# Kernel optimization log

Hardware: AMD Instinct MI355X
Metric: run time of the kernel (lower is better)

Reference implementation:

```python
import jax, jax.numpy as jnp
import numpy as np
from jax import lax

EPS = 1e-5
NUM_GROUPS = 32
OFFSET_SCALE = 1.0
K = 3            # deformable conv kernel size
KK = K * K
DWK = 7          # depthwise kernel size for offset predictor


def group_norm(x, gamma, beta, num_groups=NUM_GROUPS):
    B, C, H, W = x.shape
    xg = x.reshape(B, num_groups, C // num_groups, H, W)
    m = xg.mean(axis=(2, 3, 4), keepdims=True)
    v = xg.var(axis=(2, 3, 4), keepdims=True)
    xn = ((xg - m) * lax.rsqrt(v + EPS)).reshape(B, C, H, W)
    return xn * gamma[None, :, None, None] + beta[None, :, None, None]


def bilinear_gather(x, py, px):
    # x: [B,C,H,W]; py, px: [B,KK,H,W] absolute sample coords -> [B,C,KK,H,W]
    B, C, H, W = x.shape
    y0 = jnp.floor(py)
    x0 = jnp.floor(px)
    wy1 = py - y0
    wx1 = px - x0
    wy0 = 1.0 - wy1
    wx0 = 1.0 - wx1
    xf = x.reshape(B, C, H * W)

    def gather(yi, xi):
        valid = (yi >= 0) & (yi <= H - 1) & (xi >= 0) & (xi <= W - 1)
        yc = jnp.clip(yi, 0, H - 1).astype(jnp.int32)
        xc = jnp.clip(xi, 0, W - 1).astype(jnp.int32)
        idx = (yc * W + xc).reshape(B, -1)                      # [B, KK*H*W]
        g = jax.vmap(lambda a, i: a[:, i])(xf, idx)             # [B, C, KK*H*W]
        g = g.reshape(B, C, KK, H, W)
        return g * valid.astype(x.dtype)[:, None]

    out = (gather(y0, x0) * (wy0 * wx0)[:, None]
           + gather(y0, x0 + 1.0) * (wy0 * wx1)[:, None]
           + gather(y0 + 1.0, x0) * (wy1 * wx0)[:, None]
           + gather(y0 + 1.0, x0 + 1.0) * (wy1 * wx1)[:, None])
    return out


def deform_conv(x, dw, pw, pwb, w, b):
    # x: [B,C,H,W]; dw: [C,1,DWK,DWK] depthwise; pw: [2*KK,C,1,1]; w: [O,C,K,K]
    B, C, H, W = x.shape
    dn = ('NCHW', 'OIHW', 'NCHW')
    f = lax.conv_general_dilated(x, dw, (1, 1), 'SAME',
                                 feature_group_count=C, dimension_numbers=dn)
    off = lax.conv_general_dilated(f, pw, (1, 1), 'SAME', dimension_numbers=dn)
    off = (off + pwb[None, :, None, None]) * OFFSET_SCALE       # [B,2*KK,H,W]
    off = off.reshape(B, KK, 2, H, W)
    ks = jnp.arange(K, dtype=x.dtype) - (K - 1) / 2             # [-1,0,1]
    ky = jnp.repeat(ks, K)                                      # [KK]
    kx = jnp.tile(ks, K)
    yy, xx = jnp.meshgrid(jnp.arange(H, dtype=x.dtype),
                          jnp.arange(W, dtype=x.dtype), indexing='ij')
    py = yy[None, None] + ky[None, :, None, None] + off[:, :, 0]  # [B,KK,H,W]
    px = xx[None, None] + kx[None, :, None, None] + off[:, :, 1]
    sampled = bilinear_gather(x, py, px)                        # [B,C,KK,H,W]
    O = w.shape[0]
    out = jnp.einsum('bckhw,ock->bohw', sampled, w.reshape(O, C, KK))
    return out + b[None, :, None, None]


def setup_inputs() -> dict:
    key = jax.random.key(0)
    ks = jax.random.split(key, 10)
    B, C, H, W = 4, 256, 64, 64
    O = C
    x = jax.random.normal(ks[0], (B, C, H, W), dtype=jnp.float32)

    def conv_w(k, shape, fan_in):
        return jax.random.normal(k, shape, dtype=jnp.float32) / np.sqrt(fan_in)

    inp = {
        'x': x,
        'gn1_g': jnp.ones((C,), jnp.float32), 'gn1_b': jnp.zeros((C,), jnp.float32),
        'dw1': conv_w(ks[1], (C, 1, DWK, DWK), DWK * DWK),
        'pw1': jax.random.normal(ks[2], (2 * KK, C, 1, 1), jnp.float32) * 0.01,
        'pwb1': jnp.zeros((2 * KK,), jnp.float32),
        'w1': conv_w(ks[3], (O, C, K, K), C * KK),
        'b1': jnp.zeros((O,), jnp.float32),
        'gn2_g': jnp.ones((O,), jnp.float32), 'gn2_b': jnp.zeros((O,), jnp.float32),
        'dw2': conv_w(ks[4], (O, 1, DWK, DWK), DWK * DWK),
        'pw2': jax.random.normal(ks[5], (2 * KK, O, 1, 1), jnp.float32) * 0.01,
        'pwb2': jnp.zeros((2 * KK,), jnp.float32),
        'w2': conv_w(ks[6], (O, O, K, K), O * KK),
        'b2': jnp.zeros((O,), jnp.float32),
    }
    return inp


def reference(x, gn1_g, gn1_b, dw1, pw1, pwb1, w1, b1,
              gn2_g, gn2_b, dw2, pw2, pwb2, w2, b2):
    h = jax.nn.relu(group_norm(x, gn1_g, gn1_b))
    h = deform_conv(h, dw1, pw1, pwb1, w1, b1)
    h = jax.nn.relu(group_norm(h, gn2_g, gn2_b))
    # Dropout / DropPath are identity in eval mode
    h = deform_conv(h, dw2, pw2, pwb2, w2, b2)
    return h + x  # shortcut is Identity (in_channels == out_channels)
```

## Files before the change

kernel.cpp:

```cpp
#include <hip/hip_runtime.h>

#define B_    4
#define C_    256
#define H_    64
#define W_    64
#define HW_   4096
#define NG_   32
#define CPG_  8
#define KK_   9
#define NOFF_ 18

typedef __attribute__((ext_vector_type(8))) short short8;
typedef __attribute__((ext_vector_type(4))) short short4v;
typedef __attribute__((ext_vector_type(4))) float floatx4;
typedef __attribute__((ext_vector_type(16))) float floatx16;

static __device__ __forceinline__ short f2bf(float f) {
    union { float f; unsigned u; } v; v.f = f;
    unsigned r = v.u + 0x7fff + ((v.u >> 16) & 1);
    return (short)(r >> 16);
}
static __device__ __forceinline__ float bf2f(short s) {
    union { unsigned u; float f; } v;
    v.u = ((unsigned)(unsigned short)s) << 16;
    return v.f;
}
static __device__ __forceinline__ unsigned pkbf(float lo, float hi) {
    unsigned r;
    asm("v_cvt_pk_bf16_f32 %0, %1, %2" : "=v"(r) : "v"(lo), "v"(hi));
    return r;
}

__global__ __launch_bounds__(1024) void gn_relu_f32_kernel(
    const float* __restrict__ in, const float* __restrict__ gamma,
    const float* __restrict__ beta, short* __restrict__ outb)
{
    int b = blockIdx.x >> 5;
    int g = blockIdx.x & 31;
    const int N = CPG_ * HW_;
    size_t base = ((size_t)(b * C_ + g * CPG_)) * HW_;
    const float4* in4 = (const float4*)(in + base);
    int t = threadIdx.x;

    float s = 0.f, ss = 0.f;
    for (int i = t; i < N / 4; i += 1024) {
        float4 v = in4[i];
        s  += v.x + v.y + v.z + v.w;
        ss += v.x * v.x + v.y * v.y + v.z * v.z + v.w * v.w;
    }
    #pragma unroll
    for (int off = 32; off > 0; off >>= 1) {
        s  += __shfl_down(s, off, 64);
        ss += __shfl_down(ss, off, 64);
    }
    __shared__ float red[32];
    __shared__ float sh_rs, sh_m;
    int wid = t >> 6;
    if ((t & 63) == 0) { red[wid] = s; red[16 + wid] = ss; }
    __syncthreads();
    if (t == 0) {
        float S = 0.f, SS = 0.f;
        #pragma unroll
        for (int i = 0; i < 16; ++i) { S += red[i]; SS += red[16 + i]; }
        float m = S / (float)N;
        float var = SS / (float)N - m * m;
        sh_rs = rsqrtf(var + 1e-5f);
        sh_m = m;
    }
    __syncthreads();
    float rs = sh_rs, m = sh_m;
    short4v* out4 = (short4v*)(outb + base);
    for (int i = t; i < N / 4; i += 1024) {
        int ch = g * CPG_ + (i >> 10);
        float ga = gamma[ch] * rs;
        float be = beta[ch] - m * ga;
        float4 v = in4[i];
        short4v o;
        o.x = f2bf(fmaxf(fmaf(v.x, ga, be), 0.f));
        o.y = f2bf(fmaxf(fmaf(v.y, ga, be), 0.f));
        o.z = f2bf(fmaxf(fmaf(v.z, ga, be), 0.f));
        o.w = f2bf(fmaxf(fmaf(v.w, ga, be), 0.f));
        out4[i] = o;
    }
}

__global__ __launch_bounds__(1024) void gn_relu_bf16_kernel(
    const short* __restrict__ in, const float* __restrict__ gamma,
    const float* __restrict__ beta, short* __restrict__ outb)
{
    int b = blockIdx.x >> 5;
    int g = blockIdx.x & 31;
    const int N = CPG_ * HW_;
    size_t base = ((size_t)(b * C_ + g * CPG_)) * HW_;
    const short4v* in4 = (const short4v*)(in + base);
    int t = threadIdx.x;

    float s = 0.f, ss = 0.f;
    for (int i = t; i < N / 4; i += 1024) {
        short4v sv = in4[i];
        float vx = bf2f(sv.x), vy = bf2f(sv.y), vz = bf2f(sv.z), vw = bf2f(sv.w);
        s  += vx + vy + vz + vw;
        ss += vx * vx + vy * vy + vz * vz + vw * vw;
    }
    #pragma unroll
    for (int off = 32; off > 0; off >>= 1) {
        s  += __shfl_down(s, off, 64);
        ss += __shfl_down(ss, off, 64);
    }
    __shared__ float red[32];
    __shared__ float sh_rs, sh_m;
    int wid = t >> 6;
    if ((t & 63) == 0) { red[wid] = s; red[16 + wid] = ss; }
    __syncthreads();
    if (t == 0) {
        float S = 0.f, SS = 0.f;
        #pragma unroll
        for (int i = 0; i < 16; ++i) { S += red[i]; SS += red[16 + i]; }
        float m = S / (float)N;
        float var = SS / (float)N - m * m;
        sh_rs = rsqrtf(var + 1e-5f);
        sh_m = m;
    }
    __syncthreads();
    float rs = sh_rs, m = sh_m;
    short4v* out4 = (short4v*)(outb + base);
    for (int i = t; i < N / 4; i += 1024) {
        int ch = g * CPG_ + (i >> 10);
        float ga = gamma[ch] * rs;
        float be = beta[ch] - m * ga;
        short4v sv = in4[i];
        short4v o;
        o.x = f2bf(fmaxf(fmaf(bf2f(sv.x), ga, be), 0.f));
        o.y = f2bf(fmaxf(fmaf(bf2f(sv.y), ga, be), 0.f));
        o.z = f2bf(fmaxf(fmaf(bf2f(sv.z), ga, be), 0.f));
        o.w = f2bf(fmaxf(fmaf(bf2f(sv.w), ga, be), 0.f));
        out4[i] = o;
    }
}

__global__ __launch_bounds__(256) void dw7t_tr_kernel(
    const short* __restrict__ in,
    const float* __restrict__ dwk,
    short* __restrict__ fdwt,
    short* __restrict__ ht)
{
    __shared__ __align__(16) char smem[78112];
    int t = threadIdx.x;
    int blk = blockIdx.x;
    if (blk < 256) {
        short (*tile)[38][72] = (short(*)[38][72])smem;
        float (*wk8)[49]      = (float(*)[49])(smem + 43776);
        short (*outs)[2048]   = (short(*)[2048])(smem + 45344);
        int b = blk >> 6, o8 = (blk >> 1) & 31, rh = blk & 1;
        int c0 = o8 * 8;
        unsigned* tz = (unsigned*)smem;
        for (int i = t; i < 10944; i += 256) tz[i] = 0u;
        for (int i = t; i < 392; i += 256)
            wk8[i / 49][i % 49] = dwk[(c0 + i / 49) * 49 + (i % 49)];
        __syncthreads();
        for (int ch = 0; ch < 8; ++ch) {
            const short* src = in + ((size_t)(b * C_ + c0 + ch)) * HW_;
            for (int i = t; i < 608; i += 256) {
                int rr = i >> 4, xq = i & 15;
                int ry = rh * 32 + rr - 3;
                if (ry >= 0 && ry < 64) {
                    short4v v = *(const short4v*)(src + ry * 64 + xq * 4);
                    *(short4v*)&tile[ch][rr][4 + xq * 4] = v;
                }
            }
        }
        __syncthreads();
        for (int it = 0; it < 16; ++it) {
            int q = it * 256 + t;
            int ch = q >> 9, y = (q >> 4) & 31, x0 = (q & 15) << 2;
            float a0 = 0.f, a1 = 0.f, a2 = 0.f, a3 = 0.f;
            const float* wr0 = wk8[ch];
            #pragma unroll
            for (int dy = 0; dy < 7; ++dy) {
                const short* trw = &tile[ch][y + dy][x0];
                short4v s0 = *(const short4v*)trw;
                short4v s1 = *(const short4v*)(trw + 4);
                short4v s2 = *(const short4v*)(trw + 8);
                float r[12] = {bf2f(s0.x), bf2f(s0.y), bf2f(s0.z), bf2f(s0.w),
                               bf2f(s1.x), bf2f(s1.y), bf2f(s1.z), bf2f(s1.w),
                               bf2f(s2.x), bf2f(s2.y), bf2f(s2.z), bf2f(s2.w)};
                const float* wr = wr0 + dy * 7;
                #pragma unroll
                for (int dx = 0; dx < 7; ++dx) {
                    float wv = wr[dx];
                    a0 = fmaf(r[dx + 1], wv, a0);
                    a1 = fmaf(r[dx + 2], wv, a1);
                    a2 = fmaf(r[dx + 3], wv, a2);
                    a3 = fmaf(r[dx + 4], wv, a3);
                }
            }
            short4v o;
            o.x = f2bf(a0); o.y = f2bf(a1); o.z = f2bf(a2); o.w = f2bf(a3);
            *(short4v*)&outs[ch][y * 64 + x0] = o;
        }
        __syncthreads();
        for (int it = 0; it < 8; ++it) {
            int p = it * 256 + t;
            short8 v;
            #pragma unroll
            for (int ch = 0; ch < 8; ++ch) v[ch] = outs[ch][p];
            *(short8*)(fdwt + (((size_t)(b * 64 + rh * 32 + (p >> 6)) * 32 + o8) * 64
                               + (p & 63)) * 8) = v;
        }
    } else {
        unsigned* ltile = (unsigned*)smem;
        int q0 = blk - 256;
        int q = ((q0 & 7) << 5) | (q0 >> 3);
        int b = q >> 6;
        int px0 = (q & 63) * 64;
        const short* sb = in + (size_t)b * C_ * HW_;
        int pq4 = t & 15, cphi = t >> 4;
        #pragma unroll
        for (int i = 0; i < 8; ++i) {
            int cp = i * 16 + cphi;
            const short* r0 = sb + (size_t)(2 * cp) * HW_ + px0 + pq4 * 4;
            short4v lo = *(const short4v*)r0;
            short4v hi = *(const short4v*)(r0 + HW_);
            #pragma unroll
            for (int j = 0; j < 4; ++j) {
                int pl = pq4 * 4 + j;
                unsigned wrd = (unsigned)(unsigned short)lo[j]
                             | ((unsigned)(unsigned short)hi[j] << 16);
                ltile[pl * 132 + (cp ^ ((pl & 7) << 2))] = wrd;
            }
        }
        __syncthreads();
        int co = t & 31, ph2 = t >> 5;
        #pragma unroll
        for (int r = 0; r < 8; ++r) {
            int pl = r * 8 + ph2;
            uint4 v = *(const uint4*)&ltile[pl * 132 + ((co * 4) ^ ((pl & 7) << 2))];
            *(uint4*)(ht + ((size_t)b * HW_ + px0 + pl) * C_ + co * 8) = v;
        }
    }
}

__global__ __launch_bounds__(256) void wpack_all_kernel(
    const float* __restrict__ w1, const float* __restrict__ w2,
    const float* __restrict__ pw1, const float* __restrict__ pw2,
    short* __restrict__ wp1, short* __restrict__ wp2,
    short* __restrict__ ppk1, short* __restrict__ ppk2)
{
    int blk = blockIdx.x;
    if (blk < 4608) {
        const float* w = (blk < 2304) ? w1 : w2;
        short* wp = (blk < 2304) ? wp1 : wp2;
        int idx = (blk % 2304) * 256 + threadIdx.x;
        int j    = idx & 7;
        int lane = (idx >> 3) & 63;
        int ot   = (idx >> 9) & 7;
        int slab = idx >> 12;
        int g = slab >> 4, cc16 = slab & 15;
        int o = ot * 32 + (lane & 31);
        int c = cc16 * 16 + (lane >> 5) * 8 + j;
        wp[idx] = f2bf(w[(size_t)(o * C_ + c) * KK_ + g]);
    } else {
        int q = blk - 4608;
        const float* pw = (q < 32) ? pw1 : pw2;
        short* ppk = (q < 32) ? ppk1 : ppk2;
        int idx = (q & 31) * 256 + threadIdx.x;
        int j = idx & 7, lane = (idx >> 3) & 63;
        int ot = (idx >> 9) & 1, sl = idx >> 10;
        int o = ot * 16 + (lane & 15);
        int k = sl * 32 + (lane >> 4) * 8 + j;
        ppk[idx] = (o < NOFF_) ? f2bf(pw[o * C_ + k]) : (short)0;
    }
}

__global__ __launch_bounds__(512, 4) void deform_fused_kernel(
    const short* __restrict__ ht,   const short* __restrict__ fdw,
    const short* __restrict__ ppk,  const float* __restrict__ pwb,
    const short* __restrict__ wp,   const float* __restrict__ bias,
    const float* __restrict__ resid, float* __restrict__ outf,
    short* __restrict__ outb)
{
    int lb = ((blockIdx.x & 7) << 6) | (blockIdx.x >> 3);
    int b = lb >> 7;
    int row = (lb >> 1) & 63;
    int ph = lb & 1;
    __shared__ int   i00[288], i01[288], i10[288], i11[288];
    __shared__ float c00[288], c01[288], c10[288], c11[288];
    __shared__ __align__(16) short sbuf[2][8192];
    float* off_lds = (float*)&sbuf[0][0];
    int t = threadIdx.x;
    int wv = t >> 6, lane = t & 63;
    int pq = lane >> 4, pr = lane & 15;
    int l31 = lane & 31, hi = lane >> 5;

    if (wv < 4) {
        int ot = wv & 1, ptw = wv >> 1;
        int pxl = ptw * 16 + pr;
        int px = ph * 32 + pxl;
        const short8* fdw8 = (const short8*)fdw;
        size_t fbase = ((size_t)(b * 64 + row)) * 32;
        const short8* ap = (const short8*)ppk;
        floatx4 pacc = (floatx4){0.f, 0.f, 0.f, 0.f};
        #pragma unroll
        for (int sl = 0; sl < 8; ++sl) {
            short8 af = ap[(sl * 2 + ot) * 64 + lane];
            short8 bf = fdw8[(fbase + sl * 4 + pq) * 64 + px];
            pacc = __builtin_amdgcn_mfma_f32_16x16x32_bf16(af, bf, pacc, 0, 0, 0);
        }
        #pragma unroll
        for (int r = 0; r < 4; ++r) {
            int o = ot * 16 + pq * 4 + r;
            if (o < NOFF_) off_lds[o * 32 + pxl] = pacc[r] + pwb[o];
        }
    }
    __syncthreads();

    if (t < 288) {
        int k = t >> 5, p = t & 31;
        float offy = off_lds[(2 * k) * 32 + p];
        float offx = off_lds[(2 * k + 1) * 32 + p];
        float py = (float)row + (float)(k / 3 - 1) + offy;
        float px = (float)(ph * 32 + p) + (float)(k % 3 - 1) + offx;
        float y0f = floorf(py), x0f = floorf(px);
        float wy1 = py - y0f, wx1 = px - x0f;
        float wy0 = 1.f - wy1, wx0 = 1.f - wx1;
        float y1f = y0f + 1.f, x1f = x0f + 1.f;
        bool vy0 = (y0f >= 0.f) && (y0f <= 63.f);
        bool vy1 = (y1f >= 0.f) && (y1f <= 63.f);
        bool vx0 = (x0f >= 0.f) && (x0f <= 63.f);
        bool vx1 = (x1f >= 0.f) && (x1f <= 63.f);
        int iy0 = (int)fminf(fmaxf(y0f, 0.f), 63.f);
        int iy1 = (int)fminf(fmaxf(y1f, 0.f), 63.f);
        int ix0 = (int)fminf(fmaxf(x0f, 0.f), 63.f);
        int ix1 = (int)fminf(fmaxf(x1f, 0.f), 63.f);
        i00[t] = iy0 * 64 + ix0; i01[t] = iy0 * 64 + ix1;
        i10[t] = iy1 * 64 + ix0; i11[t] = iy1 * 64 + ix1;
        c00[t] = (vy0 && vx0) ? wy0 * wx0 : 0.f;
        c01[t] = (vy0 && vx1) ? wy0 * wx1 : 0.f;
        c10[t] = (vy1 && vx0) ? wy1 * wx0 : 0.f;
        c11[t] = (vy1 && vx1) ? wy1 * wx1 : 0.f;
    }
    __syncthreads();

    int c8a = t & 7;
    int pan = (t >> 3) & 1;
    int spx = t >> 4;
    const short* hb0 = ht + ((size_t)b * HW_) * C_ + pan * 128 + c8a * 8;
    const short* hb1 = hb0 + 64;
    int oct0 = pan * 16 + c8a;
    int oct1 = oct0 + 8;
    int slotA = ((oct0 & 16) | ((oct0 ^ spx) & 15)) * 8;
    int slotB = ((oct1 & 16) | ((oct1 ^ spx) & 15)) * 8;
    int srow = spx * 256;

    short8 ra[4], rb[4];
    auto prefetch = [&](int g) {
        int e = g * 32 + spx;
        int a00 = i00[e], a01 = i01[e], a10 = i10[e], a11 = i11[e];
        ra[0] = *(const short8*)(hb0 + (size_t)a00 * C_);
        ra[1] = *(const short8*)(hb0 + (size_t)a01 * C_);
        ra[2] = *(const short8*)(hb0 + (size_t)a10 * C_);
        ra[3] = *(const short8*)(hb0 + (size_t)a11 * C_);
        rb[0] = *(const short8*)(hb1 + (size_t)a00 * C_);
        rb[1] = *(const short8*)(hb1 + (size_t)a01 * C_);
        rb[2] = *(const short8*)(hb1 + (size_t)a10 * C_);
        rb[3] = *(const short8*)(hb1 + (size_t)a11 * C_);
    };
    auto stage_write = [&](int g, int bi) {
        int e = g * 32 + spx;
        float w00 = c00[e], w01 = c01[e], w10 = c10[e], w11 = c11[e];
        uint4 va, vb;
        float f0, f1;
        #define BLEND(R, J) (w00 * bf2f(R[0][J]) + w01 * bf2f(R[1][J]) \
                           + w10 * bf2f(R[2][J]) + w11 * bf2f(R[3][J]))
        f0 = BLEND(ra, 0); f1 = BLEND(ra, 1); va.x = pkbf(f0, f1);
        f0 = BLEND(ra, 2); f1 = BLEND(ra, 3); va.y = pkbf(f0, f1);
        f0 = BLEND(ra, 4); f1 = BLEND(ra, 5); va.z = pkbf(f0, f1);
        f0 = BLEND(ra, 6); f1 = BLEND(ra, 7); va.w = pkbf(f0, f1);
        f0 = BLEND(rb, 0); f1 = BLEND(rb, 1); vb.x = pkbf(f0, f1);
        f0 = BLEND(rb, 2); f1 = BLEND(rb, 3); vb.y = pkbf(f0, f1);
        f0 = BLEND(rb, 4); f1 = BLEND(rb, 5); vb.z = pkbf(f0, f1);
        f0 = BLEND(rb, 6); f1 = BLEND(rb, 7); vb.w = pkbf(f0, f1);
        #undef BLEND
        short* sp = &sbuf[bi][srow];
        *(uint4*)&sp[slotA] = va;
        *(uint4*)&sp[slotB] = vb;
    };

    int pairId = wv;

    floatx16 acc;
    #pragma unroll
    for (int i = 0; i < 16; ++i) acc[i] = 0.f;

    prefetch(0);
    stage_write(0, 0);
    prefetch(1);
    __syncthreads();

    const short8* wp8 = (const short8*)wp;

    for (int g = 0; g < 9; ++g) {
        const short* sb = &sbuf[g & 1][0];
        #pragma unroll
        for (int q4 = 0; q4 < 4; ++q4) {
            short8 af[4];
            #pragma unroll
            for (int qq = 0; qq < 4; ++qq)
                af[qq] = wp8[(size_t)(((g * 16 + q4 * 4 + qq) * 8 + pairId) * 64 + lane)];
            #pragma unroll
            for (int qq = 0; qq < 4; ++qq) {
                int s = q4 * 4 + qq;
                int oct = s * 2 + hi;
                int so = ((oct & 16) | ((oct ^ l31) & 15)) << 3;
                short8 b0 = *(const short8*)&sb[l31 * 256 + so];
                acc = __builtin_amdgcn_mfma_f32_32x32x16_bf16(af[qq], b0, acc, 0, 0, 0);
            }
        }
        if (g + 1 < 9) {
            stage_write(g + 1, (g + 1) & 1);
            if (g + 2 < 9) prefetch(g + 2);
        }
        __syncthreads();
    }

    #pragma unroll
    for (int r = 0; r < 16; ++r) {
        int o = pairId * 32 + (r & 3) + 8 * (r >> 2) + 4 * hi;
        float v = acc[r] + bias[o];
        size_t ob = ((size_t)(b * C_ + o)) * HW_ + row * 64 + ph * 32 + l31;
        if (outf) {
            if (resid) v += resid[ob];
            outf[ob] = v;
        } else {
            outb[ob] = f2bf(v);
        }
    }
}

extern "C" void kernel_launch(void* const* d_in, const int* in_sizes, int n_in,
                              void* d_out, int out_size, void* d_ws, size_t ws_size,
                              hipStream_t stream)
{
    const float* x     = (const float*)d_in[0];
    const float* gn1_g = (const float*)d_in[1];
    const float* gn1_b = (const float*)d_in[2];
    const float* dw1   = (const float*)d_in[3];
    const float* pw1   = (const float*)d_in[4];
    const float* pwb1  = (const float*)d_in[5];
    const float* w1    = (const float*)d_in[6];
    const float* b1    = (const float*)d_in[7];
    const float* gn2_g = (const float*)d_in[8];
    const float* gn2_b = (const float*)d_in[9];
    const float* dw2   = (const float*)d_in[10];
    const float* pw2   = (const float*)d_in[11];
    const float* pwb2  = (const float*)d_in[12];
    const float* w2    = (const float*)d_in[13];
    const float* b2    = (const float*)d_in[14];
    float* out = (float*)d_out;

    float* ws   = (float*)d_ws;
    short* y1b  = (short*)ws;
    short* hbf  = (short*)(ws + 2097152);
    short* hbt  = (short*)(ws + 4194304);
    short* fdwt = (short*)(ws + 8388608);
    short* wp1  = (short*)(ws + 10485760);
    short* wp2  = (short*)(ws + 10780672);
    short* ppk1 = (short*)(ws + 11075584);
    short* ppk2 = (short*)(ws + 11079680);

    wpack_all_kernel<<<4672, 256, 0, stream>>>(w1, w2, pw1, pw2,
                                               wp1, wp2, ppk1, ppk2);

    gn_relu_f32_kernel<<<B_ * NG_, 1024, 0, stream>>>(x, gn1_g, gn1_b, hbf);
    dw7t_tr_kernel<<<512, 256, 0, stream>>>(hbf, dw1, fdwt, hbt);
    deform_fused_kernel<<<512, 512, 0, stream>>>(
        hbt, fdwt, ppk1, pwb1, wp1, b1, nullptr, nullptr, y1b);

    gn_relu_bf16_kernel<<<B_ * NG_, 1024, 0, stream>>>(y1b, gn2_g, gn2_b, hbf);
    dw7t_tr_kernel<<<512, 256, 0, stream>>>(hbf, dw2, fdwt, hbt);
    deform_fused_kernel<<<512, 512, 0, stream>>>(
        hbt, fdwt, ppk2, pwb2, wp2, b2, x, out, nullptr);
}
```

Measured before the change: 256.1 us.

## Process full image row per block with 2x2 MFMA tiles and split-K reduction

Each deform-conv block now covers a whole 64-pixel row with 1024 threads instead of half a row with 512. Waves split into 4 output-channel groups by 4 K-slab groups, and each wave computes a 2x2 grid of 32x32 MFMA tiles, so weight and sampled-feature fragments are reused across tiles. Partial sums from the K groups are combined through LDS in a tree reduction before the final store. This is meant to halve weight traffic per pixel and raise MFMA reuse, at the cost of doubled LDS use, four accumulator tiles per wave (register pressure), extra barriers for the reduction, and only 256 blocks in the grid.

```diff
diff --git a/kernel.cpp b/kernel.cpp
--- a/kernel.cpp
+++ b/kernel.cpp
@@ -272,30 +272,28 @@
     }
 }
 
-__global__ __launch_bounds__(512, 4) void deform_fused_kernel(
+__global__ __launch_bounds__(1024, 4) void deform_fused_kernel(
     const short* __restrict__ ht,   const short* __restrict__ fdw,
     const short* __restrict__ ppk,  const float* __restrict__ pwb,
     const short* __restrict__ wp,   const float* __restrict__ bias,
     const float* __restrict__ resid, float* __restrict__ outf,
     short* __restrict__ outb)
 {
-    int lb = ((blockIdx.x & 7) << 6) | (blockIdx.x >> 3);
-    int b = lb >> 7;
-    int row = (lb >> 1) & 63;
-    int ph = lb & 1;
-    __shared__ int   i00[288], i01[288], i10[288], i11[288];
-    __shared__ float c00[288], c01[288], c10[288], c11[288];
-    __shared__ __align__(16) short sbuf[2][8192];
+    int lb = ((blockIdx.x & 7) << 5) | (blockIdx.x >> 3);
+    int b = lb >> 6;
+    int row = lb & 63;
+    __shared__ int   i00[576], i01[576], i10[576], i11[576];
+    __shared__ float c00[576], c01[576], c10[576], c11[576];
+    __shared__ __align__(16) short sbuf[2][16384];
     float* off_lds = (float*)&sbuf[0][0];
     int t = threadIdx.x;
     int wv = t >> 6, lane = t & 63;
     int pq = lane >> 4, pr = lane & 15;
     int l31 = lane & 31, hi = lane >> 5;
 
-    if (wv < 4) {
+    if (wv < 8) {
         int ot = wv & 1, ptw = wv >> 1;
-        int pxl = ptw * 16 + pr;
-        int px = ph * 32 + pxl;
+        int px = ptw * 16 + pr;
         const short8* fdw8 = (const short8*)fdw;
         size_t fbase = ((size_t)(b * 64 + row)) * 32;
         const short8* ap = (const short8*)ppk;
@@ -309,17 +307,18 @@
         #pragma unroll
         for (int r = 0; r < 4; ++r) {
             int o = ot * 16 + pq * 4 + r;
-            if (o < NOFF_) off_lds[o * 32 + pxl] = pacc[r] + pwb[o];
-        }
-    }
-    __syncthreads();
-
-    if (t < 288) {
-        int k = t >> 5, p = t & 31;
-        float offy = off_lds[(2 * k) * 32 + p];
-        float offx = off_lds[(2 * k + 1) * 32 + p];
+            if (o < NOFF_) off_lds[o * 64 + px] = pacc[r] + pwb[o];
+        }
+    }
+    __syncthreads();
+
+    if (t < 576) {
+        int e = t;
+        int k = e >> 6, p = e & 63;
+        float offy = off_lds[(2 * k) * 64 + p];
+        float offx = off_lds[(2 * k + 1) * 64 + p];
         float py = (float)row + (float)(k / 3 - 1) + offy;
-        float px = (float)(ph * 32 + p) + (float)(k % 3 - 1) + offx;
+        float px = (float)p   + (float)(k % 3 - 1) + offx;
         float y0f = floorf(py), x0f = floorf(px);
         float wy1 = py - y0f, wx1 = px - x0f;
         float wy0 = 1.f - wy1, wx0 = 1.f - wx1;
@@ -332,12 +331,12 @@
         int iy1 = (int)fminf(fmaxf(y1f, 0.f), 63.f);
         int ix0 = (int)fminf(fmaxf(x0f, 0.f), 63.f);
         int ix1 = (int)fminf(fmaxf(x1f, 0.f), 63.f);
-        i00[t] = iy0 * 64 + ix0; i01[t] = iy0 * 64 + ix1;
-        i10[t] = iy1 * 64 + ix0; i11[t] = iy1 * 64 + ix1;
-        c00[t] = (vy0 && vx0) ? wy0 * wx0 : 0.f;
-        c01[t] = (vy0 && vx1) ? wy0 * wx1 : 0.f;
-        c10[t] = (vy1 && vx0) ? wy1 * wx0 : 0.f;
-        c11[t] = (vy1 && vx1) ? wy1 * wx1 : 0.f;
+        i00[e] = iy0 * 64 + ix0; i01[e] = iy0 * 64 + ix1;
+        i10[e] = iy1 * 64 + ix0; i11[e] = iy1 * 64 + ix1;
+        c00[e] = (vy0 && vx0) ? wy0 * wx0 : 0.f;
+        c01[e] = (vy0 && vx1) ? wy0 * wx1 : 0.f;
+        c10[e] = (vy1 && vx0) ? wy1 * wx0 : 0.f;
+        c11[e] = (vy1 && vx1) ? wy1 * wx1 : 0.f;
     }
     __syncthreads();
 
@@ -354,7 +353,7 @@
 
     short8 ra[4], rb[4];
     auto prefetch = [&](int g) {
-        int e = g * 32 + spx;
+        int e = g * 64 + spx;
         int a00 = i00[e], a01 = i01[e], a10 = i10[e], a11 = i11[e];
         ra[0] = *(const short8*)(hb0 + (size_t)a00 * C_);
         ra[1] = *(const short8*)(hb0 + (size_t)a01 * C_);
@@ -366,7 +365,7 @@
         rb[3] = *(const short8*)(hb1 + (size_t)a11 * C_);
     };
     auto stage_write = [&](int g, int bi) {
-        int e = g * 32 + spx;
+        int e = g * 64 + spx;
         float w00 = c00[e], w01 = c01[e], w10 = c10[e], w11 = c11[e];
         uint4 va, vb;
         float f0, f1;
@@ -386,11 +385,15 @@
         *(uint4*)&sp[slotB] = vb;
     };
 
-    int pairId = wv;
-
-    floatx16 acc;
+    int oq = wv & 3;
+    int kq = wv >> 2;
+
+    floatx16 acc[2][2];
     #pragma unroll
-    for (int i = 0; i < 16; ++i) acc[i] = 0.f;
+    for (int i = 0; i < 16; ++i) {
+        acc[0][0][i] = 0.f; acc[0][1][i] = 0.f;
+        acc[1][0][i] = 0.f; acc[1][1][i] = 0.f;
+    }
 
     prefetch(0);
     stage_write(0, 0);
@@ -402,19 +405,18 @@
     for (int g = 0; g < 9; ++g) {
         const short* sb = &sbuf[g & 1][0];
         #pragma unroll
-        for (int q4 = 0; q4 < 4; ++q4) {
-            short8 af[4];
-            #pragma unroll
-            for (int qq = 0; qq < 4; ++qq)
-                af[qq] = wp8[(size_t)(((g * 16 + q4 * 4 + qq) * 8 + pairId) * 64 + lane)];
-            #pragma unroll
-            for (int qq = 0; qq < 4; ++qq) {
-                int s = q4 * 4 + qq;
-                int oct = s * 2 + hi;
-                int so = ((oct & 16) | ((oct ^ l31) & 15)) << 3;
-                short8 b0 = *(const short8*)&sb[l31 * 256 + so];
-                acc = __builtin_amdgcn_mfma_f32_32x32x16_bf16(af[qq], b0, acc, 0, 0, 0);
-            }
+        for (int s4 = 0; s4 < 4; ++s4) {
+            int slab = kq * 4 + s4;
+            short8 a0 = wp8[(size_t)(((g * 16 + slab) * 8 + 2 * oq) * 64 + lane)];
+            short8 a1 = wp8[(size_t)(((g * 16 + slab) * 8 + 2 * oq + 1) * 64 + lane)];
+            int oct = slab * 2 + hi;
+            int so = ((oct & 16) | ((oct ^ l31) & 15)) << 3;
+            short8 b0 = *(const short8*)&sb[l31 * 256 + so];
+            short8 b1 = *(const short8*)&sb[(32 + l31) * 256 + so];
+            acc[0][0] = __builtin_amdgcn_mfma_f32_32x32x16_bf16(a0, b0, acc[0][0], 0, 0, 0);
+            acc[0][1] = __builtin_amdgcn_mfma_f32_32x32x16_bf16(a0, b1, acc[0][1], 0, 0, 0);
+            acc[1][0] = __builtin_amdgcn_mfma_f32_32x32x16_bf16(a1, b0, acc[1][0], 0, 0, 0);
+            acc[1][1] = __builtin_amdgcn_mfma_f32_32x32x16_bf16(a1, b1, acc[1][1], 0, 0, 0);
         }
         if (g + 1 < 9) {
             stage_write(g + 1, (g + 1) & 1);
@@ -423,16 +425,64 @@
         __syncthreads();
     }
 
-    #pragma unroll
-    for (int r = 0; r < 16; ++r) {
-        int o = pairId * 32 + (r & 3) + 8 * (r >> 2) + 4 * hi;
-        float v = acc[r] + bias[o];
-        size_t ob = ((size_t)(b * C_ + o)) * HW_ + row * 64 + ph * 32 + l31;
-        if (outf) {
-            if (resid) v += resid[ob];
-            outf[ob] = v;
-        } else {
-            outb[ob] = f2bf(v);
+    float* xf = (float*)&sbuf[0][0];
+    auto wr4 = [&](int reg) {
+        float* bp = xf + reg * 4096;
+        #pragma unroll
+        for (int a = 0; a < 4; ++a) {
+            #pragma unroll
+            for (int q = 0; q < 4; ++q) {
+                floatx4 v = {acc[a >> 1][a & 1][q * 4 + 0], acc[a >> 1][a & 1][q * 4 + 1],
+                             acc[a >> 1][a & 1][q * 4 + 2], acc[a >> 1][a & 1][q * 4 + 3]};
+                *(floatx4*)&bp[a * 1024 + q * 256 + lane * 4] = v;
+            }
+        }
+    };
+    auto rd4 = [&](int reg) {
+        float* bp = xf + reg * 4096;
+        #pragma unroll
+        for (int a = 0; a < 4; ++a) {
+            #pragma unroll
+            for (int q = 0; q < 4; ++q) {
+                floatx4 v = *(const floatx4*)&bp[a * 1024 + q * 256 + lane * 4];
+                acc[a >> 1][a & 1][q * 4 + 0] += v.x;
+                acc[a >> 1][a & 1][q * 4 + 1] += v.y;
+                acc[a >> 1][a & 1][q * 4 + 2] += v.z;
+                acc[a >> 1][a & 1][q * 4 + 3] += v.w;
+            }
+        }
+    };
+    if (kq == 1) wr4(oq);
+    __syncthreads();
+    if (kq == 0) rd4(oq);
+    __syncthreads();
+    if (kq == 3) wr4(oq);
+    __syncthreads();
+    if (kq == 2) rd4(oq);
+    __syncthreads();
+    if (kq == 2) wr4(oq);
+    __syncthreads();
+    if (kq == 0) rd4(oq);
+
+    if (kq == 0) {
+        #pragma unroll
+        for (int oi = 0; oi < 2; ++oi) {
+            #pragma unroll
+            for (int r = 0; r < 16; ++r) {
+                int o = oq * 64 + oi * 32 + (r & 3) + 8 * (r >> 2) + 4 * hi;
+                float bo = bias[o];
+                float v0 = acc[oi][0][r] + bo;
+                float v1 = acc[oi][1][r] + bo;
+                size_t ob = ((size_t)(b * C_ + o)) * HW_ + row * 64 + l31;
+                if (outf) {
+                    if (resid) { v0 += resid[ob]; v1 += resid[ob + 32]; }
+                    outf[ob] = v0;
+                    outf[ob + 32] = v1;
+                } else {
+                    outb[ob] = f2bf(v0);
+                    outb[ob + 32] = f2bf(v1);
+                }
+            }
         }
     }
 }
@@ -473,11 +523,11 @@
 
     gn_relu_f32_kernel<<<B_ * NG_, 1024, 0, stream>>>(x, gn1_g, gn1_b, hbf);
     dw7t_tr_kernel<<<512, 256, 0, stream>>>(hbf, dw1, fdwt, hbt);
-    deform_fused_kernel<<<512, 512, 0, stream>>>(
+    deform_fused_kernel<<<B_ * H_, 1024, 0, stream>>>(
         hbt, fdwt, ppk1, pwb1, wp1, b1, nullptr, nullptr, y1b);
 
     gn_relu_bf16_kernel<<<B_ * NG_, 1024, 0, stream>>>(y1b, gn2_g, gn2_b, hbf);
     dw7t_tr_kernel<<<512, 256, 0, stream>>>(hbf, dw2, fdwt, hbt);
-    deform_fused_kernel<<<512, 512, 0, stream>>>(
+    deform_fused_kernel<<<B_ * H_, 1024, 0, stream>>>(
         hbt, fdwt, ppk2, pwb2, wp2, b2, x, out, nullptr);
 }
```

Measured after the change: 277.1 us. +8.2%, slower.
